# Kernel tuning notes

Measured on AMD Instinct MI355X. Metric: run time of the kernel, lower is better.

## Reference

```python
import jax, jax.numpy as jnp
import numpy as np

EPS = 1e-4
SILU_GAIN = 1.0 / 0.596  # magnitude-preserving SiLU gain
SCALES = (4, 4, 8)       # prod == A_DIM == 128
T = 0.3                  # residual lerp weight


def mp_silu(x):
    return jax.nn.silu(x) * SILU_GAIN


def pixel_norm(x):
    # normalize over channel dim (axis=1) to unit RMS
    return x * jax.lax.rsqrt(jnp.mean(jnp.square(x), axis=1, keepdims=True) + EPS)


def norm_w(w):
    # magnitude-preserving conv: per-output-filter L2-normalized weight
    n = jnp.sqrt(jnp.sum(jnp.square(w), axis=tuple(range(1, w.ndim)), keepdims=True) + 1e-8)
    return w / n


def mp_add(a, b, t=T):
    return (a * (1.0 - t) + b * t) / np.sqrt((1.0 - t) ** 2 + t ** 2)


def conv2d(x, w, groups=1, padding=((0, 0), (0, 0))):
    return jax.lax.conv_general_dilated(
        x, w, (1, 1), padding,
        dimension_numbers=('NCHW', 'OIHW', 'NCHW'), feature_group_count=groups)


def conv1d(x, w, groups=1, padding=((0, 0),)):
    return jax.lax.conv_general_dilated(
        x, w, (1,), padding,
        dimension_numbers=('NCH', 'OIH', 'NCH'), feature_group_count=groups)


def avgpool_freq(x, s):
    B, C, F, L = x.shape
    return jnp.mean(x.reshape(B, C, F // s, s, L), axis=3)


def min_gru(h, w):
    # minGRU: z_t = sigmoid(Wz h_t), c_t = Wc h_t, s_t = (1-z_t) s_{t-1} + z_t c_t
    z, c = jnp.split(conv1d(h, norm_w(w)), 2, axis=1)
    z = jax.nn.sigmoid(z)
    a, b = 1.0 - z, z * c  # linear recurrence s_t = a_t s_{t-1} + b_t

    def comb(x, y):
        a1, b1 = x
        a2, b2 = y
        return a2 * a1, a2 * b1 + b2

    _, out = jax.lax.associative_scan(comb, (a, b), axis=-1)
    return out


def conv_block(x, w1, wd, w2, wdn, s):
    # x: [B, d, F, L]
    x = pixel_norm(x)
    r = mp_silu(x)
    r = conv2d(r, norm_w(w1))                                            # d -> h, 1x1
    r = conv2d(r, norm_w(wd), groups=wd.shape[0], padding=((2, 2), (1, 1)))  # depthwise 5x3
    r = mp_silu(r)
    r = conv2d(r, norm_w(w2))                                            # h -> d, 1x1
    h = mp_add(x, r)
    return conv2d(avgpool_freq(h, s), norm_w(wdn))                       # d -> 2d, freq /s


def seq_block(x, hg_w, dw_w, gru_w, out_w):
    # x: [B, d, L]
    x = pixel_norm(x)
    h, g = jnp.split(conv1d(x, norm_w(hg_w)), 2, axis=1)  # each [B, H, L]
    h = mp_silu(h)
    h = conv1d(h, norm_w(dw_w), groups=dw_w.shape[0], padding=((1, 1),))  # depthwise k=3
    h = mp_silu(h)
    h = min_gru(h, gru_w)
    h = h * mp_silu(g)
    return mp_add(x, conv1d(h, norm_w(out_w)))


def setup_inputs() -> dict:
    key = jax.random.key(0)
    ks = jax.random.split(key, 18)
    rn = lambda k, s: jax.random.normal(k, s, dtype=jnp.float32)
    B, L, A = 2, 2048, 128
    return {
        'audio': rn(ks[0], (B, A, L)),
        'proj_w': rn(ks[1], (64, 1, 1, 1)) * 0.5,
        'proj_b': jnp.zeros((64,), jnp.float32),
        'c0_w1': rn(ks[2], (128, 64, 1, 1)),
        'c0_wd': rn(ks[3], (128, 1, 5, 3)),
        'c0_w2': rn(ks[4], (64, 128, 1, 1)),
        'c0_dn': rn(ks[5], (128, 64, 1, 1)),
        'c1_w1': rn(ks[6], (256, 128, 1, 1)),
        'c1_wd': rn(ks[7], (256, 1, 5, 3)),
        'c1_w2': rn(ks[8], (128, 256, 1, 1)),
        'c1_dn': rn(ks[9], (256, 128, 1, 1)),
        'c2_w1': rn(ks[10], (512, 256, 1, 1)),
        'c2_wd': rn(ks[11], (512, 1, 5, 3)),
        'c2_w2': rn(ks[12], (256, 512, 1, 1)),
        'c2_dn': rn(ks[13], (512, 256, 1, 1)),
        'hg_w': rn(ks[14], (4, 2048, 512, 1)),
        'dw_w': rn(ks[15], (4, 1024, 1, 3)),
        'gru_w': rn(ks[16], (4, 2048, 1024, 1)),
        'out_w': rn(ks[17], (4, 512, 1024, 1)),
    }


def reference(audio, proj_w, proj_b,
              c0_w1, c0_wd, c0_w2, c0_dn,
              c1_w1, c1_wd, c1_w2, c1_dn,
              c2_w1, c2_wd, c2_w2, c2_dn,
              hg_w, dw_w, gru_w, out_w):
    h = audio[:, None]  # [B, 1, A_DIM, L]
    h = conv2d(h, proj_w) + proj_b[None, :, None, None]
    blocks = ((c0_w1, c0_wd, c0_w2, c0_dn),
              (c1_w1, c1_wd, c1_w2, c1_dn),
              (c2_w1, c2_wd, c2_w2, c2_dn))
    for (w1, wd, w2, dn), s in zip(blocks, SCALES):
        h = conv_block(h, w1, wd, w2, dn, s)
    h = h[:, :, 0, :]  # freq dim reduced to 1 -> [B, dim, L]
    for i in range(hg_w.shape[0]):
        h = seq_block(h, hg_w[i], dw_w[i], gru_w[i], out_w[i])
    return mp_silu(h)
```

## Files before the change

### kernel.cpp

```cpp
#include <hip/hip_runtime.h>
#include <math.h>

#define GAIN 1.6778523489932886f
#define MPS  1.3130643285972254f

typedef __attribute__((ext_vector_type(8))) short short8;
typedef __attribute__((ext_vector_type(4))) short short4v;
typedef __attribute__((ext_vector_type(4))) float float4v;

__device__ __forceinline__ float silu_g(float x){
  float s = 1.0f/(1.0f + __expf(-x));
  return x*s*GAIN;
}
__device__ __forceinline__ short f2bf(float f){
  unsigned u = __builtin_bit_cast(unsigned, f);
  u += 0x7fffu + ((u >> 16) & 1u);
  return (short)(u >> 16);
}
__device__ __forceinline__ float bf2f(unsigned short h){
  return __builtin_bit_cast(float, ((unsigned)h) << 16);
}

typedef __attribute__((address_space(3))) unsigned int as3_uint;
typedef const __attribute__((address_space(1))) unsigned int as1_cuint;
__device__ __forceinline__ void gload16(const unsigned short* gsrc, unsigned short* ldst){
  __builtin_amdgcn_global_load_lds((as1_cuint*)gsrc, (as3_uint*)ldst, 16, 0, 0);
}

struct NcEnt { const float* w; int O, K, dstOff; };
struct NcArgs { NcEnt e[16]; };

__global__ __launch_bounds__(64) void normcast_kernel(NcArgs na, unsigned short* __restrict__ wbf){
  int row = blockIdx.x;
  int base = 0; int i;
  for (i = 0; i < 16; i++){
    if (row < base + na.e[i].O) break;
    base += na.e[i].O;
  }
  if (i >= 16) return;
  int r = row - base; int K = na.e[i].K;
  const float* w = na.e[i].w + (long)r*K;
  unsigned short* dst = wbf + na.e[i].dstOff + (long)r*K;
  int tid = threadIdx.x;
  float s = 0.f;
  const bool v4 = ((K & 3) == 0);
  if (v4){
    for (int k = tid*4; k < K; k += 256){
      float4v v = *(const float4v*)&w[k];
      s += v[0]*v[0] + v[1]*v[1] + v[2]*v[2] + v[3]*v[3];
    }
  } else {
    for (int k = tid; k < K; k += 64){ float v = w[k]; s += v*v; }
  }
  for (int off = 32; off; off >>= 1) s += __shfl_down(s, off);
  float inv = rsqrtf(__shfl(s, 0) + 1e-8f);
  if (v4){
    for (int k = tid*4; k < K; k += 256){
      float4v v = *(const float4v*)&w[k];
      short4v o = { f2bf(v[0]*inv), f2bf(v[1]*inv), f2bf(v[2]*inv), f2bf(v[3]*inv) };
      *(short4v*)&dst[k] = o;
    }
  } else {
    for (int k = tid; k < K; k += 64) dst[k] = (unsigned short)f2bf(w[k]*inv);
  }
}

__global__ __launch_bounds__(64) void projstats_kernel(const float* __restrict__ pw, const float* __restrict__ pb,
                                                       float* __restrict__ S){
  int t = threadIdx.x;
  float p = pw[t], q = pb[t];
  float s1 = p*p, s2 = p*q, s3 = q*q;
  for (int off = 32; off; off >>= 1){
    s1 += __shfl_down(s1, off); s2 += __shfl_down(s2, off); s3 += __shfl_down(s3, off);
  }
  if (t == 0){ S[0] = s1; S[1] = s2; S[2] = s3; }
}

__global__ __launch_bounds__(256) void invn_audio_kernel(const float* __restrict__ audio, const float* __restrict__ S,
                                                         float* __restrict__ invn){
  long i = blockIdx.x*256 + threadIdx.x;
  if (i >= (2L*128*2048)/4) return;
  long e = i*4;
  float S1 = S[0], S2 = S[1], S3 = S[2];
  float4v a = *(const float4v*)&audio[e];
  float4v o;
  #pragma unroll
  for (int j = 0; j < 4; j++) o[j] = rsqrtf((a[j]*a[j]*S1 + 2.f*a[j]*S2 + S3)/64.f + 1e-4f);
  *(float4v*)&invn[e] = o;
}

template<int G, bool BF>
__global__ __launch_bounds__(256) void invn_reduce_kernel(const void* __restrict__ Xv, float* __restrict__ invn,
                                                          int C, int F){
  constexpr int L = 256/G;
  int t = threadIdx.x; int cs = t / L; int li = t % L;
  long pos = (long)blockIdx.x*L + li;
  int bf = (int)(pos >> 11); int l = (int)(pos & 2047);
  int b = bf / F; int f = bf - b*F;
  long base = ((long)b*C*F + f)*2048 + l;
  long stride = (long)F*2048;
  float s = 0.f;
  if (BF){
    const unsigned short* X = (const unsigned short*)Xv;
    for (int c = cs; c < C; c += G){ float v = bf2f(X[base + (long)c*stride]); s += v*v; }
  } else {
    const float* X = (const float*)Xv;
    for (int c = cs; c < C; c += G){ float v = X[base + (long)c*stride]; s += v*v; }
  }
  __shared__ float red[256];
  red[t] = s; __syncthreads();
  #pragma unroll
  for (int off = G/2; off > 0; off >>= 1){
    if (cs < off) red[t] += red[t + off*L];
    __syncthreads();
  }
  if (cs == 0) invn[pos] = rsqrtf(red[li]/(float)C + 1e-4f);
}

template<bool SILU, bool BF>
__global__ __launch_bounds__(256) void applynorm_kernel(const void* __restrict__ Xv, const float* __restrict__ invn,
                                                        unsigned short* __restrict__ XB, int C, int F, long total4){
  long i = blockIdx.x*256 + threadIdx.x;
  if (i >= total4) return;
  long e = i*4;
  int l = (int)(e & 2047); long r = e >> 11;
  int f = (int)(r % F); long bc = r / F; int b = (int)(bc / C);
  float4v x;
  if (BF){
    short4v u = *(const short4v*)((const unsigned short*)Xv + e);
    x = (float4v){ bf2f((unsigned short)u[0]), bf2f((unsigned short)u[1]),
                   bf2f((unsigned short)u[2]), bf2f((unsigned short)u[3]) };
  } else {
    x = *(const float4v*)((const float*)Xv + e);
  }
  float4v iv = *(const float4v*)&invn[((long)b*F + f)*2048 + l];
  short4v o;
  #pragma unroll
  for (int j = 0; j < 4; j++){
    float v = x[j]*iv[j];
    o[j] = f2bf(SILU ? silu_g(v) : v);
  }
  *(short4v*)&XB[e] = o;
}

__global__ __launch_bounds__(256) void normT_kernel(const float* __restrict__ SEQ,
                                                    const float* __restrict__ invn,
                                                    unsigned short* __restrict__ XST){
  __shared__ float tile[64][65];
  const int l0 = blockIdx.x*64, c0 = blockIdx.y*64, b = blockIdx.z;
  const int t = threadIdx.x;
  const int lr = (t & 15)*4;
  const int cr = t >> 4;
  #pragma unroll
  for (int p = 0; p < 4; p++){
    int c = cr + p*16;
    float4v v = *(const float4v*)&SEQ[((long)(b*512 + c0 + c))*2048 + l0 + lr];
    tile[c][lr+0] = v[0]; tile[c][lr+1] = v[1]; tile[c][lr+2] = v[2]; tile[c][lr+3] = v[3];
  }
  __syncthreads();
  const int cc = (t & 7)*8;
  const int lw = t >> 3;
  #pragma unroll
  for (int p = 0; p < 2; p++){
    int l = lw + p*32;
    float iv = invn[b*2048 + l0 + l];
    short8 o;
    #pragma unroll
    for (int j = 0; j < 8; j++) o[j] = f2bf(tile[cc+j][l] * iv);
    *(short8*)&XST[((long)(b*2048 + l0 + l))*512 + c0 + cc] = o;
  }
}

struct GTArgs {
  const unsigned short* A;
  const unsigned short* B;
  unsigned short* O1;
  unsigned short* O2;
  int N, K;
};

template<int EMODE>
__global__ __launch_bounds__(256,2) void gemmT_kernel(GTArgs g){
  __shared__ __align__(16) char SMEMraw[49152];
  unsigned short (*Asm)[4096] = (unsigned short (*)[4096])SMEMraw;
  unsigned short (*Bsm)[4096] = (unsigned short (*)[4096])(SMEMraw + 24576);
  const int t = threadIdx.x;
  const int lane = t & 63;
  const int wc = (t >> 7) & 1;
  const int wsd = (t >> 6) & 1;
  const int q = lane >> 4, r16 = lane & 15;
  const int m0 = blockIdx.x * 128;
  const int n0 = blockIdx.y * 128;
  const int K = g.K;

  const int r0 = t >> 2;
  const int c8 = (((t & 3) ^ ((r0 >> 1) & 3)) << 3);
  const unsigned short* Ap = g.A + (long)(n0 + r0)*K + c8;
  const unsigned short* Bp = g.B + (long)(m0 + r0)*K + c8;

  auto stage = [&](int bi, int k0){
    gload16(Ap + k0,           &Asm[bi][t*8]);
    gload16(Ap + 64*K + k0,    &Asm[bi][2048 + t*8]);
    gload16(Bp + k0,           &Bsm[bi][t*8]);
    gload16(Bp + 64*K + k0,    &Bsm[bi][2048 + t*8]);
  };

  float4v acc[4][4];
  #pragma unroll
  for (int i = 0; i < 4; i++)
    #pragma unroll
    for (int j = 0; j < 4; j++) acc[i][j] = (float4v){0.f,0.f,0.f,0.f};

  const int nit = K >> 5;
  stage(0, 0);
  stage(1, 32);

  const int qsw = ((q ^ ((r16 >> 1) & 3)) << 3);

  for (int it = 0; it < nit; ++it){
    if (it + 2 < nit){
      stage((it + 2) % 3, (it + 2) << 5);
      asm volatile("" ::: "memory");
      asm volatile("s_waitcnt vmcnt(8)" ::: "memory");
    } else if (it + 1 < nit){
      asm volatile("s_waitcnt vmcnt(4)" ::: "memory");
    } else {
      asm volatile("s_waitcnt vmcnt(0)" ::: "memory");
    }
    __builtin_amdgcn_s_barrier();
    asm volatile("" ::: "memory");

    const unsigned short* As = Asm[it % 3];
    const unsigned short* Bs = Bsm[it % 3];
    short8 afr[4], bfr[4];
    #pragma unroll
    for (int i = 0; i < 4; i++) afr[i] = *(const short8*)&As[(wc*64 + i*16 + r16)*32 + qsw];
    #pragma unroll
    for (int j = 0; j < 4; j++) bfr[j] = *(const short8*)&Bs[(wsd*64 + j*16 + r16)*32 + qsw];
    #pragma unroll
    for (int i = 0; i < 4; i++)
      #pragma unroll
      for (int j = 0; j < 4; j++)
        acc[i][j] = __builtin_amdgcn_mfma_f32_16x16x32_bf16(afr[i], bfr[j], acc[i][j], 0, 0, 0);

    asm volatile("" ::: "memory");
    __builtin_amdgcn_s_barrier();
  }

  if (EMODE == 1 && n0 < 1024){
    float* Cf = (float*)SMEMraw;
    #pragma unroll
    for (int h = 0; h < 2; h++){
      __syncthreads();
      if (wc == h){
        #pragma unroll
        for (int j = 0; j < 4; j++){
          int m = wsd*64 + j*16 + r16;
          #pragma unroll
          for (int i = 0; i < 4; i++)
            *(float4v*)&Cf[m*68 + i*16 + q*4] = acc[i][j];
        }
      }
      __syncthreads();
      #pragma unroll
      for (int p = 0; p < 4; p++){
        int m = (t >> 3) + p*32;
        int n8 = (t & 7)*8;
        int gm = m0 + m; int b = gm >> 11, l = gm & 2047;
        float4v v0 = *(const float4v*)&Cf[m*68 + n8];
        float4v v1 = *(const float4v*)&Cf[m*68 + n8 + 4];
        short8 o;
        #pragma unroll
        for (int e = 0; e < 4; e++){ o[e] = f2bf(silu_g(v0[e])); o[e+4] = f2bf(silu_g(v1[e])); }
        *(short8*)&g.O1[((long)(b*2048 + l))*1024 + (n0 + h*64 + n8)] = o;
      }
    }
  } else {
    float* Csm = (float*)SMEMraw;
    #pragma unroll
    for (int qtr = 0; qtr < 4; qtr++){
      __syncthreads();
      if (wc == (qtr >> 1)){
        #pragma unroll
        for (int ii = 0; ii < 2; ii++){
          int i = (qtr & 1)*2 + ii;
          #pragma unroll
          for (int j = 0; j < 4; j++){
            int m = wsd*64 + j*16 + r16;
            #pragma unroll
            for (int rg = 0; rg < 4; rg++)
              Csm[(ii*16 + q*4 + rg)*132 + m] = acc[i][j][rg];
          }
        }
      }
      __syncthreads();
      #pragma unroll
      for (int sp = 0; sp < 2; sp++){
        int nrow = (t >> 4) + sp*16;
        int n = n0 + qtr*32 + nrow;
        int m8 = (t & 15)*8;
        int gm = m0 + m8; int b = gm >> 11, l = gm & 2047;
        float4v v0 = *(const float4v*)&Csm[nrow*132 + m8];
        float4v v1 = *(const float4v*)&Csm[nrow*132 + m8 + 4];
        short8 o;
        #pragma unroll
        for (int e = 0; e < 4; e++){ o[e] = f2bf(v0[e]); o[e+4] = f2bf(v1[e]); }
        if (EMODE == 1) *(short8*)&g.O2[((long)(b*1024 + (n - 1024)))*2048 + l] = o;
        else            *(short8*)&g.O1[((long)(b*2048 + n))*2048 + l] = o;
      }
    }
  }
}

struct GemmArgs {
  const unsigned short* A;
  const unsigned short* Bh;
  const float* invn; const float* audio;
  const float* pw; const float* pb;
  const unsigned short* auxXH;
  unsigned short* CoutH; unsigned short* Cout2H;
  int N, K, Fdim, Lw, lq0, BLw, Bl0, CLw, Cl0, Nsto, Fsrc;
};

template<int BMODE, int EMODE>
__global__ __launch_bounds__(256,2) void mgemm_kernel(GemmArgs g){
  __shared__ __align__(16) char SMEMraw[20480];
  unsigned short* Asm = (unsigned short*)SMEMraw;
  unsigned short* Bsm = Asm + 128*40;
  const int t = threadIdx.x;
  const int lane = t & 63;
  const int wave = t >> 6;
  const int wc = wave >> 1, wsd = wave & 1;
  const int q = lane >> 4, r16 = lane & 15;
  const int s0 = blockIdx.x * 128;
  const int n0 = blockIdx.y * 128;
  const int FL = g.Fdim * g.Lw;

  const int ar = t >> 1, ah = t & 1;
  const int an = n0 + ar;
  const bool aval = an < g.N;
  const unsigned short* Aptr = g.A + (long)an*g.K + ah*16;

  const int kg = t & 7, mg = t >> 3;
  const int mb = s0 + mg*4;
  int bcol = mb / FL; int rr = mb - bcol*FL;
  int fcol = (g.Fdim > 1) ? (rr / g.Lw) : 0;
  int labs = g.lq0 + (rr - fcol*g.Lw);
  const bool cv = (bcol < 2);
  bool lv[4];
  #pragma unroll
  for (int j = 0; j < 4; j++) lv[j] = cv && (labs + j >= 0) && (labs + j < 2048);
  const bool vec4 = cv && (labs >= 0) && (labs + 3 < 2048);
  const unsigned short* bbase = g.Bh;
  if (cv) bbase = g.Bh + ((long)(bcol*g.K)*g.Fsrc + fcol)*g.BLw + (labs - g.Bl0);
  const long kstep = (long)g.Fsrc * g.BLw;

  float invn4[4] = {0,0,0,0}, aud4[4] = {0,0,0,0};
  if (BMODE == 2){
    #pragma unroll
    for (int j = 0; j < 4; j++) if (lv[j]){
      invn4[j] = g.invn[(bcol*g.Fdim + fcol)*2048 + labs + j];
      aud4[j]  = g.audio[(bcol*128 + fcol)*2048 + labs + j];
    }
  }

  float4v acc[4][4];
  #pragma unroll
  for (int i = 0; i < 4; i++)
    #pragma unroll
    for (int j = 0; j < 4; j++) acc[i][j] = (float4v){0.f,0.f,0.f,0.f};

  short8 pa0 = {0,0,0,0,0,0,0,0}, pa1 = {0,0,0,0,0,0,0,0};
  short4v praw[4];
  #pragma unroll
  for (int i = 0; i < 4; i++) praw[i] = (short4v){0,0,0,0};

  auto ldA = [&](int kb){
    if (aval){
      pa0 = *(const short8*)(Aptr + kb);
      pa1 = *(const short8*)(Aptr + kb + 8);
    }
  };
  auto ldB = [&](int kb){
    #pragma unroll
    for (int i = 0; i < 4; i++){
      const int k = kb + kg*4 + i;
      const unsigned short* bp = bbase + (long)k*kstep;
      if (vec4) praw[i] = *(const short4v*)bp;
      else {
        short4v u = {0,0,0,0};
        #pragma unroll
        for (int j = 0; j < 4; j++) if (lv[j]) u[j] = (short)bp[j];
        praw[i] = u;
      }
    }
  };

  ldA(0);
  if (BMODE == 0) ldB(0);

  for (int k0 = 0; k0 < g.K; k0 += 32){
    short8 sa0 = pa0, sa1 = pa1;
    short4v bpk[4];
    if (BMODE == 0){
      #pragma unroll
      for (int j = 0; j < 4; j++){
        short4v p;
        #pragma unroll
        for (int i = 0; i < 4; i++) p[i] = praw[i][j];
        bpk[j] = p;
      }
    } else {
      float tv[4][4];
      #pragma unroll
      for (int i = 0; i < 4; i++){
        const int k = k0 + kg*4 + i;
        const float pwk = g.pw[k], pbk = g.pb[k];
        #pragma unroll
        for (int j = 0; j < 4; j++) tv[i][j] = lv[j] ? silu_g((aud4[j]*pwk + pbk)*invn4[j]) : 0.f;
      }
      #pragma unroll
      for (int j = 0; j < 4; j++){
        short4v p;
        #pragma unroll
        for (int i = 0; i < 4; i++) p[i] = f2bf(tv[i][j]);
        bpk[j] = p;
      }
    }
    if (k0 + 32 < g.K){
      ldA(k0 + 32);
      if (BMODE == 0) ldB(k0 + 32);
    }

    __syncthreads();
    *(short8*)&Asm[ar*40 + ah*16]     = sa0;
    *(short8*)&Asm[ar*40 + ah*16 + 8] = sa1;
    #pragma unroll
    for (int j = 0; j < 4; j++)
      *(short4v*)&Bsm[(mg*4 + j)*40 + kg*4] = bpk[j];
    __syncthreads();

    short8 afr[4], bfr[4];
    #pragma unroll
    for (int i = 0; i < 4; i++) afr[i] = *(const short8*)&Asm[(wc*64 + i*16 + r16)*40 + q*8];
    #pragma unroll
    for (int j = 0; j < 4; j++) bfr[j] = *(const short8*)&Bsm[(wsd*64 + j*16 + r16)*40 + q*8];
    #pragma unroll
    for (int i = 0; i < 4; i++)
      #pragma unroll
      for (int j = 0; j < 4; j++)
        acc[i][j] = __builtin_amdgcn_mfma_f32_16x16x32_bf16(afr[i], bfr[j], acc[i][j], 0, 0, 0);
  }

  {
    float* Csm = (float*)SMEMraw;
    #pragma unroll
    for (int qtr = 0; qtr < 4; qtr++){
      __syncthreads();
      if (wc == (qtr >> 1)){
        #pragma unroll
        for (int ii = 0; ii < 2; ii++){
          int i = (qtr & 1)*2 + ii;
          #pragma unroll
          for (int j = 0; j < 4; j++){
            int m = wsd*64 + j*16 + r16;
            #pragma unroll
            for (int rg = 0; rg < 4; rg++)
              Csm[(ii*16 + q*4 + rg)*132 + m] = acc[i][j][rg];
          }
        }
      }
      __syncthreads();
      #pragma unroll
      for (int sp = 0; sp < 2; sp++){
        int nrow = (t >> 4) + sp*16;
        int n = n0 + qtr*32 + nrow;
        int m8 = (t & 15)*8;
        if (n >= g.N) continue;
        int sg = s0 + m8;
        int b2 = sg / FL; int r2 = sg - b2*FL;
        if (b2 >= 2) continue;
        int f2 = (g.Fdim > 1) ? (r2 / g.Lw) : 0;
        int l2 = g.lq0 + (r2 - f2*g.Lw);
        float4v v0 = *(const float4v*)&Csm[nrow*132 + m8];
        float4v v1 = *(const float4v*)&Csm[nrow*132 + m8 + 4];
        long obase = ((long)(b2*g.Nsto + n)*g.Fdim + f2)*g.CLw + (l2 - g.Cl0);
        short8 o;
        if (EMODE == 1){
          #pragma unroll
          for (int e = 0; e < 4; e++){ o[e] = f2bf(v0[e]); o[e+4] = f2bf(v1[e]); }
        } else if (EMODE == 2){
          short8 axv = *(const short8*)&g.auxXH[((long)(b2*g.N + n)*g.Fdim + f2)*2048 + l2];
          const float* ivp = &g.invn[(b2*g.Fdim + f2)*2048 + l2];
          float4v iv0 = *(const float4v*)ivp;
          float4v iv1 = *(const float4v*)(ivp + 4);
          #pragma unroll
          for (int e = 0; e < 4; e++){
            float xn0 = bf2f((unsigned short)axv[e]) * iv0[e];
            float xn1 = bf2f((unsigned short)axv[e+4]) * iv1[e];
            o[e]   = f2bf((xn0*0.7f + v0[e]*0.3f)*MPS);
            o[e+4] = f2bf((xn1*0.7f + v1[e]*0.3f)*MPS);
          }
        } else {
          float pwn = g.pw[n], pbn = g.pb[n];
          const float* ap  = &g.audio[(b2*128 + f2)*2048 + l2];
          const float* ivp = &g.invn[(b2*g.Fdim + f2)*2048 + l2];
          float4v a0 = *(const float4v*)ap,  a1 = *(const float4v*)(ap + 4);
          float4v iv0 = *(const float4v*)ivp, iv1 = *(const float4v*)(ivp + 4);
          #pragma unroll
          for (int e = 0; e < 4; e++){
            float xn0 = (a0[e]*pwn + pbn)*iv0[e];
            float xn1 = (a1[e]*pwn + pbn)*iv1[e];
            o[e]   = f2bf((xn0*0.7f + v0[e]*0.3f)*MPS);
            o[e+4] = f2bf((xn1*0.7f + v1[e]*0.3f)*MPS);
          }
        }
        *(short8*)&g.CoutH[obase] = o;
      }
    }
  }
}

struct DnArgs {
  const unsigned short* A; const unsigned short* P;
  float* Cout; unsigned short* CoutH;
  int N, K, F2, Lc, l0;
};

template<int EMODE>
__global__ __launch_bounds__(256,4) void mgemm64_kernel(DnArgs g){
  __shared__ __align__(16) char SMEM[10240];
  unsigned short* Asm = (unsigned short*)SMEM;
  unsigned short* Bsm = Asm + 64*40;
  const int t = threadIdx.x;
  const int lane = t & 63;
  const int wave = t >> 6;
  const int wc = wave >> 1, wsd = wave & 1;
  const int q = lane >> 4, r16 = lane & 15;
  const int s0 = blockIdx.x * 64;
  const int n0 = blockIdx.y * 64;
  const int FL = g.F2 * g.Lc;

  const int ar = t >> 2, ah = t & 3;
  const unsigned short* Aptr = g.A + (long)(n0 + ar)*g.K + ah*8;
  const int kg = t & 7, mg = t >> 3;
  const bool bstage = (mg < 16);
  const int mb = s0 + (mg & 15)*4;
  const int bcol = mb / FL; const int rr = mb - bcol*FL;
  const int fcol = rr / g.Lc; const int li = rr - fcol*g.Lc;
  const unsigned short* bbase = g.P + ((long)(bcol*g.K)*g.F2 + fcol)*g.Lc + li;
  const long kstep = (long)g.F2 * g.Lc;

  float4v acc[2][2];
  #pragma unroll
  for (int i = 0; i < 2; i++)
    #pragma unroll
    for (int j = 0; j < 2; j++) acc[i][j] = (float4v){0.f,0.f,0.f,0.f};

  short8 pa = {0,0,0,0,0,0,0,0};
  short4v praw[4];
  #pragma unroll
  for (int i = 0; i < 4; i++) praw[i] = (short4v){0,0,0,0};

  auto ldA = [&](int kb){ pa = *(const short8*)(Aptr + kb); };
  auto ldB = [&](int kb){
    if (bstage){
      #pragma unroll
      for (int i = 0; i < 4; i++)
        praw[i] = *(const short4v*)(bbase + (long)(kb + kg*4 + i)*kstep);
    }
  };
  ldA(0); ldB(0);

  for (int k0 = 0; k0 < g.K; k0 += 32){
    short8 sa = pa;
    short4v bpk[4];
    #pragma unroll
    for (int j = 0; j < 4; j++){
      short4v p;
      #pragma unroll
      for (int i = 0; i < 4; i++) p[i] = praw[i][j];
      bpk[j] = p;
    }
    if (k0 + 32 < g.K){ ldA(k0 + 32); ldB(k0 + 32); }

    __syncthreads();
    *(short8*)&Asm[ar*40 + ah*8] = sa;
    if (bstage){
      #pragma unroll
      for (int j = 0; j < 4; j++)
        *(short4v*)&Bsm[((mg & 15)*4 + j)*40 + kg*4] = bpk[j];
    }
    __syncthreads();

    short8 afr[2], bfr[2];
    #pragma unroll
    for (int i = 0; i < 2; i++) afr[i] = *(const short8*)&Asm[(wc*32 + i*16 + r16)*40 + q*8];
    #pragma unroll
    for (int j = 0; j < 2; j++) bfr[j] = *(const short8*)&Bsm[(wsd*32 + j*16 + r16)*40 + q*8];
    #pragma unroll
    for (int i = 0; i < 2; i++)
      #pragma unroll
      for (int j = 0; j < 2; j++)
        acc[i][j] = __builtin_amdgcn_mfma_f32_16x16x32_bf16(afr[i], bfr[j], acc[i][j], 0, 0, 0);
  }

  {
    float* Csm = (float*)SMEM;
    const int b2 = s0 / FL; const int r20 = s0 - b2*FL;
    const int f2c = r20 / g.Lc; const int l2c = g.l0 + (r20 - f2c*g.Lc);
    #pragma unroll
    for (int nq = 0; nq < 4; nq++){
      __syncthreads();
      if (wc == (nq >> 1)){
        const int i = nq & 1;
        #pragma unroll
        for (int j = 0; j < 2; j++)
          #pragma unroll
          for (int rg = 0; rg < 4; rg++)
            Csm[(q*4 + rg)*68 + wsd*32 + j*16 + r16] = acc[i][j][rg];
      }
      __syncthreads();
      int nrow = t >> 4;
      int mq = (t & 15)*4;
      int n = n0 + nq*16 + nrow;
      float4v v = *(const float4v*)&Csm[nrow*68 + mq];
      long oidx = ((long)(b2*g.N + n)*g.F2 + f2c)*2048 + l2c + mq;
      if (EMODE == 0){
        *(float4v*)&g.Cout[oidx] = v;
      } else {
        short4v o = { f2bf(v[0]), f2bf(v[1]), f2bf(v[2]), f2bf(v[3]) };
        *(short4v*)&g.CoutH[oidx] = o;
      }
    }
  }
}

template<int EMODE>
__global__ __launch_bounds__(256,4) void seqout_kernel(const unsigned short* __restrict__ A,
                                                       const unsigned short* __restrict__ Bh,
                                                       const float* __restrict__ invn,
                                                       const float* __restrict__ auxX,
                                                       float* __restrict__ Cout, int K){
  __shared__ __align__(16) char SMEM[10240];
  unsigned short* Asm = (unsigned short*)SMEM;
  unsigned short* Bsm = Asm + 64*40;
  const int t = threadIdx.x;
  const int lane = t & 63;
  const int wave = t >> 6;
  const int wc = wave >> 1, wsd = wave & 1;
  const int q = lane >> 4, r16 = lane & 15;
  const int s0 = blockIdx.x * 64;
  const int n0 = blockIdx.y * 64;

  const int ar = t >> 2, ah = t & 3;
  const unsigned short* Aptr = A + (long)(n0 + ar)*K + ah*8;
  const int kg = t & 7, mg = t >> 3;
  const bool bstage = (mg < 16);
  const int mb = s0 + (mg & 15)*4;
  const int bcol = mb >> 11, lb = mb & 2047;
  const unsigned short* bbase = Bh + ((long)bcol*K)*2048 + lb;

  float4v acc[2][2];
  #pragma unroll
  for (int i = 0; i < 2; i++)
    #pragma unroll
    for (int j = 0; j < 2; j++) acc[i][j] = (float4v){0.f,0.f,0.f,0.f};

  short8 pa = {0,0,0,0,0,0,0,0};
  short4v praw[4];
  #pragma unroll
  for (int i = 0; i < 4; i++) praw[i] = (short4v){0,0,0,0};

  auto ldA = [&](int kb){ pa = *(const short8*)(Aptr + kb); };
  auto ldB = [&](int kb){
    if (bstage){
      #pragma unroll
      for (int i = 0; i < 4; i++)
        praw[i] = *(const short4v*)(bbase + (long)(kb + kg*4 + i)*2048);
    }
  };
  ldA(0); ldB(0);

  for (int k0 = 0; k0 < K; k0 += 32){
    short8 sa = pa;
    short4v bpk[4];
    #pragma unroll
    for (int j = 0; j < 4; j++){
      short4v p;
      #pragma unroll
      for (int i = 0; i < 4; i++) p[i] = praw[i][j];
      bpk[j] = p;
    }
    if (k0 + 32 < K){ ldA(k0 + 32); ldB(k0 + 32); }

    __syncthreads();
    *(short8*)&Asm[ar*40 + ah*8] = sa;
    if (bstage){
      #pragma unroll
      for (int j = 0; j < 4; j++)
        *(short4v*)&Bsm[((mg & 15)*4 + j)*40 + kg*4] = bpk[j];
    }
    __syncthreads();

    short8 afr[2], bfr[2];
    #pragma unroll
    for (int i = 0; i < 2; i++) afr[i] = *(const short8*)&Asm[(wc*32 + i*16 + r16)*40 + q*8];
    #pragma unroll
    for (int j = 0; j < 2; j++) bfr[j] = *(const short8*)&Bsm[(wsd*32 + j*16 + r16)*40 + q*8];
    #pragma unroll
    for (int i = 0; i < 2; i++)
      #pragma unroll
      for (int j = 0; j < 2; j++)
        acc[i][j] = __builtin_amdgcn_mfma_f32_16x16x32_bf16(afr[i], bfr[j], acc[i][j], 0, 0, 0);
  }

  {
    float* Csm = (float*)SMEM;
    const int b2 = s0 >> 11; const int l0b = s0 & 2047;
    #pragma unroll
    for (int nq = 0; nq < 4; nq++){
      __syncthreads();
      if (wc == (nq >> 1)){
        const int i = nq & 1;
        #pragma unroll
        for (int j = 0; j < 2; j++)
          #pragma unroll
          for (int rg = 0; rg < 4; rg++)
            Csm[(q*4 + rg)*68 + wsd*32 + j*16 + r16] = acc[i][j][rg];
      }
      __syncthreads();
      int nrow = t >> 4;
      int mq = (t & 15)*4;
      int n = n0 + nq*16 + nrow;
      int l = l0b + mq;
      float4v v = *(const float4v*)&Csm[nrow*68 + mq];
      float4v ax = *(const float4v*)&auxX[((long)b2*512 + n)*2048 + l];
      float4v iv = *(const float4v*)&invn[b2*2048 + l];
      float4v r;
      #pragma unroll
      for (int e = 0; e < 4; e++){
        float xn = ax[e]*iv[e];
        float rr = (xn*0.7f + v[e]*0.3f)*MPS;
        r[e] = (EMODE == 6) ? silu_g(rr) : rr;
      }
      *(float4v*)&Cout[((long)b2*512 + n)*2048 + l] = r;
    }
  }
}

__global__ __launch_bounds__(256) void poolf_kernel(const unsigned short* __restrict__ Hb,
                                                    unsigned short* __restrict__ P,
                                                    int F2, int s, int Lc, long total4){
  long i = blockIdx.x*256 + threadIdx.x;
  if (i >= total4) return;
  long e = i*4;
  int li = (int)(e % Lc); long r0 = e / Lc;
  int f2 = (int)(r0 % F2); long r = r0 / F2;
  const unsigned short* src = Hb + ((long)r*F2*s + (long)f2*s)*Lc + li;
  float a0=0,a1=0,a2=0,a3=0;
  for (int p = 0; p < s; p++){
    short4v u = *(const short4v*)(src + (long)p*Lc);
    a0 += bf2f((unsigned short)u[0]); a1 += bf2f((unsigned short)u[1]);
    a2 += bf2f((unsigned short)u[2]); a3 += bf2f((unsigned short)u[3]);
  }
  float inv = 1.f/(float)s;
  short4v o = { f2bf(a0*inv), f2bf(a1*inv), f2bf(a2*inv), f2bf(a3*inv) };
  *(short4v*)&P[((long)r*F2 + f2)*Lc + li] = o;
}

struct DwArgs { const unsigned short* R1; const unsigned short* wd; unsigned short* R2; int C, F, Lc, l0; };
__global__ __launch_bounds__(256) void dw2d_kernel(DwArgs a){
  int idx = blockIdx.x*256 + threadIdx.x;
  int Lq = a.Lc >> 3;
  int Fq = a.F >> 2;
  int total = 2*a.C*Fq*Lq;
  if (idx >= total) return;
  int lq = idx % Lq; int r = idx / Lq;
  int fq = r % Fq; r /= Fq;
  int c = r % a.C; int b = r / a.C;
  int f0 = fq*4;
  int labs = a.l0 + lq*8;
  int Lw = a.Lc + 8;
  const unsigned short* base = a.R1 + (long)((b*a.C + c)*a.F)*Lw + (labs - (a.l0 - 4));
  const unsigned short* w = a.wd + c*15;
  float W[5][3];
  #pragma unroll
  for (int tp = 0; tp < 5; tp++)
    #pragma unroll
    for (int j = 0; j < 3; j++) W[tp][j] = bf2f(w[tp*3 + j]);

  const bool llo = (labs > 0);
  const bool lhi = (labs + 8 < 2048);
  float acc[4][8];
  #pragma unroll
  for (int t = 0; t < 4; t++)
    #pragma unroll
    for (int j = 0; j < 8; j++) acc[t][j] = 0.f;

  #pragma unroll
  for (int r8 = 0; r8 < 8; r8++){
    int rrow = f0 - 2 + r8;
    if (rrow < 0 || rrow >= a.F) continue;
    const unsigned short* p = base + (long)rrow*Lw;
    short4v u0 = *(const short4v*)p;
    short4v u1 = *(const short4v*)(p + 4);
    float x[10];
    x[0] = llo ? bf2f(p[-1]) : 0.f;
    x[1] = bf2f((unsigned short)u0[0]); x[2] = bf2f((unsigned short)u0[1]);
    x[3] = bf2f((unsigned short)u0[2]); x[4] = bf2f((unsigned short)u0[3]);
    x[5] = bf2f((unsigned short)u1[0]); x[6] = bf2f((unsigned short)u1[1]);
    x[7] = bf2f((unsigned short)u1[2]); x[8] = bf2f((unsigned short)u1[3]);
    x[9] = lhi ? bf2f(p[8]) : 0.f;
    #pragma unroll
    for (int t = 0; t < 4; t++){
      const int df = r8 - 2 - t;
      if (df < -2 || df > 2) continue;
      float w0 = W[df+2][0], w1 = W[df+2][1], w2 = W[df+2][2];
      #pragma unroll
      for (int j = 0; j < 8; j++)
        acc[t][j] += w0*x[j] + w1*x[j+1] + w2*x[j+2];
    }
  }

  unsigned short* ob = a.R2 + ((long)((b*a.C + c)*a.F + f0))*a.Lc + (labs - a.l0);
  #pragma unroll
  for (int t = 0; t < 4; t++){
    short8 o;
    #pragma unroll
    for (int j = 0; j < 8; j++) o[j] = f2bf(silu_g(acc[t][j]));
    *(short8*)(ob + (long)t*a.Lc) = o;
  }
}

__global__ __launch_bounds__(256) void dwseqT_kernel(const unsigned short* __restrict__ HST,
                                                     const unsigned short* __restrict__ w,
                                                     unsigned short* __restrict__ H2T){
  int idx = blockIdx.x*256 + threadIdx.x;
  if (idx >= 2*2048*128) return;
  int c0 = (idx & 127) * 8; long bt = idx >> 7;
  int tt = (int)(bt & 2047);
  const unsigned short* base = HST + bt*1024 + c0;
  short8 zz = {0,0,0,0,0,0,0,0};
  short8 x1 = *(const short8*)base;
  short8 x0 = (tt > 0)    ? *(const short8*)(base - 1024) : zz;
  short8 x2 = (tt < 2047) ? *(const short8*)(base + 1024) : zz;
  const unsigned short* wp = w + c0*3;
  short8 o;
  #pragma unroll
  for (int j = 0; j < 8; j++){
    float w0 = bf2f(wp[3*j]), w1 = bf2f(wp[3*j+1]), w2 = bf2f(wp[3*j+2]);
    float v = w0*bf2f((unsigned short)x0[j]) + w1*bf2f((unsigned short)x1[j]) + w2*bf2f((unsigned short)x2[j]);
    o[j] = f2bf(silu_g(v));
  }
  *(short8*)&H2T[bt*1024 + c0] = o;
}

__global__ __launch_bounds__(256) void scan_kernel(const unsigned short* __restrict__ ZC, const unsigned short* __restrict__ G,
                                                   unsigned short* __restrict__ SC){
  int bc = blockIdx.x;
  int b = bc >> 10, c = bc & 1023;
  const unsigned short* zrow = ZC + ((long)(b*2048 + c))*2048;
  const unsigned short* crow = ZC + ((long)(b*2048 + 1024 + c))*2048;
  const unsigned short* grow = G + (long)bc*2048;
  unsigned short* orow = SC + (long)bc*2048;
  int tid = threadIdx.x;
  int t0 = tid*8;
  short8 zv = *(const short8*)&zrow[t0];
  short8 cv = *(const short8*)&crow[t0];
  float av[8], bv[8];
  float A = 1.f, Bv = 0.f;
  #pragma unroll
  for (int j = 0; j < 8; j++){
    float z = bf2f((unsigned short)zv[j]); float cval = bf2f((unsigned short)cv[j]);
    float zs = 1.f/(1.f + __expf(-z));
    float a = 1.f - zs; float bb = zs*cval;
    av[j] = a; bv[j] = bb;
    Bv = a*Bv + bb;
    A = a*A;
  }
  int lane = tid & 63, wv = tid >> 6;
  float iA = A, iB = Bv;
  #pragma unroll
  for (int off = 1; off < 64; off <<= 1){
    float pA = __shfl_up(iA, off);
    float pB = __shfl_up(iB, off);
    if (lane >= off){ iB = iA*pB + iB; iA = iA*pA; }
  }
  float exA = __shfl_up(iA, 1);
  float exB = __shfl_up(iB, 1);
  if (lane == 0){ exA = 1.f; exB = 0.f; }
  __shared__ float sWA[4], sWB[4];
  if (lane == 63){ sWA[wv] = iA; sWB[wv] = iB; }
  __syncthreads();
  float wpA = 1.f, wpB = 0.f;
  #pragma unroll
  for (int w = 0; w < 3; w++){
    if (w < wv){ wpB = sWA[w]*wpB + sWB[w]; wpA = wpA*sWA[w]; }
  }
  float h = exA*wpB + exB;
  short8 gv = *(const short8*)&grow[t0];
  short8 ov;
  #pragma unroll
  for (int j = 0; j < 8; j++){
    h = av[j]*h + bv[j];
    ov[j] = f2bf(h * silu_g(bf2f((unsigned short)gv[j])));
  }
  *(short8*)&orow[t0] = ov;
}

extern "C" void kernel_launch(void* const* d_in, const int* in_sizes, int n_in,
                              void* d_out, int out_size, void* d_ws, size_t ws_size,
                              hipStream_t stream) {
  const float* audio = (const float*)d_in[0];
  const float* pw = (const float*)d_in[1];
  const float* pb = (const float*)d_in[2];
  const float* cw1[3] = {(const float*)d_in[3], (const float*)d_in[7], (const float*)d_in[11]};
  const float* cwd[3] = {(const float*)d_in[4], (const float*)d_in[8], (const float*)d_in[12]};
  const float* cw2[3] = {(const float*)d_in[5], (const float*)d_in[9], (const float*)d_in[13]};
  const float* cdn[3] = {(const float*)d_in[6], (const float*)d_in[10], (const float*)d_in[14]};
  const float* hgw  = (const float*)d_in[15];
  const float* dww  = (const float*)d_in[16];
  const float* gruw = (const float*)d_in[17];
  const float* outw = (const float*)d_in[18];
  float* out = (float*)d_out;

  char* P0 = (char*)d_ws;
  float*          INVW = (float*)P0;                    P0 += 131072;
  unsigned short* WBF  = (unsigned short*)P0;           P0 += 30443776;
  float*          INVN = (float*)P0;                    P0 += 2097152;
  char*           XBZC = P0;                            P0 += 33554432;
  unsigned short* IN1h = (unsigned short*)P0;           P0 += 33554432;
  unsigned short* IN2h = (unsigned short*)P0;           P0 += 16777216;
  float*          SEQ  = (float*)P0;                    P0 += 8388608;
  char*           ARENA = P0;
  long arenaBytes = (long)ws_size - (long)(P0 - (char*)d_ws);
  float* S = INVW + 32000;

  const float* wsrc[16] = {cw1[0],cwd[0],cw2[0],cdn[0], cw1[1],cwd[1],cw2[1],cdn[1],
                           cw1[2],cwd[2],cw2[2],cdn[2], hgw, dww, gruw, outw};
  int Os[16] = {128,128,64,128, 256,256,128,256, 512,512,256,512, 8192,4096,8192,2048};
  int Ks[16] = {64,15,128,64, 128,15,256,128, 256,15,512,256, 512,3,1024,1024};
  int wbfOff[16];
  {
    int wo = 0;
    for (int i = 0; i < 16; i++){ wbfOff[i] = wo; wo += Os[i]*Ks[i]; }
  }
  {
    NcArgs na;
    int rows = 0;
    for (int i = 0; i < 16; i++){
      na.e[i].w = wsrc[i]; na.e[i].O = Os[i]; na.e[i].K = Ks[i]; na.e[i].dstOff = wbfOff[i];
      rows += Os[i];
    }
    normcast_kernel<<<rows, 64, 0, stream>>>(na, WBF);
  }
  projstats_kernel<<<1, 64, 0, stream>>>(pw, pb, S);

  int Cin_[3]  = {64,128,256};
  int Cmid_[3] = {128,256,512};
  int F_[3]    = {128,32,8};
  int s_[3]    = {4,4,8};
  const unsigned short* XinH[3] = {nullptr, IN1h, IN2h};
  unsigned short* XoutH[3] = {IN1h, IN2h, nullptr};
  int iW1[3]={0,4,8}, iWd[3]={1,5,9}, iW2[3]={2,6,10}, iDn[3]={3,7,11};

  for (int b = 0; b < 3; b++){
    int Cin = Cin_[b], Cmid = Cmid_[b], F = F_[b], s = s_[b];
    int F2 = F/s;
    int nc = 16;
    for (int c = 1; c <= 16; c <<= 1){
      long Lc = 2048/c;
      long bytes = 2L*(2L*Cmid*F*(Lc+8) + 2L*Cmid*F*Lc + 2L*Cin*F*Lc + 2L*Cin*F2*Lc);
      if (bytes <= arenaBytes){ nc = c; break; }
    }
    int Lc = 2048/nc;
    unsigned short* R1 = (unsigned short*)ARENA;
    unsigned short* R2 = R1 + 2L*Cmid*F*(Lc+8);
    unsigned short* Hb = R2 + 2L*Cmid*F*Lc;
    unsigned short* Pb = Hb + 2L*Cin*F*Lc;
    unsigned short* XB = (unsigned short*)XBZC;

    if (b == 0){
      invn_audio_kernel<<<(2*128*2048/4+255)/256, 256, 0, stream>>>(audio, S, INVN);
    } else {
      int positions = 2*F*2048;
      invn_reduce_kernel<8,true><<<positions/32, 256, 0, stream>>>(XinH[b], INVN, Cin, F);
      long total4 = (long)2*Cin*F*2048/4;
      applynorm_kernel<true,true><<<(int)((total4+255)/256), 256, 0, stream>>>(XinH[b], INVN, XB, Cin, F, total4);
    }

    for (int ci = 0; ci < nc; ci++){
      int l0 = ci*Lc;
      GemmArgs ga{};
      ga.A = WBF + wbfOff[iW1[b]];
      ga.Bh = XB; ga.invn = INVN; ga.audio = audio; ga.pw = pw; ga.pb = pb;
      ga.CoutH = R1; ga.N = Cmid; ga.K = Cin; ga.Fdim = F; ga.Lw = Lc+8; ga.lq0 = l0-4;
      ga.BLw = 2048; ga.Bl0 = 0; ga.CLw = Lc+8; ga.Cl0 = l0-4; ga.Nsto = Cmid; ga.Fsrc = F;
      int M1 = 2*F*(Lc+8);
      dim3 g1((M1+127)/128, (Cmid+127)/128);
      if (b == 0) mgemm_kernel<2,1><<<g1,256,0,stream>>>(ga);
      else        mgemm_kernel<0,1><<<g1,256,0,stream>>>(ga);
      DwArgs da{R1, WBF + wbfOff[iWd[b]], R2, Cmid, F, Lc, l0};
      int tdw = 2*Cmid*(F/4)*(Lc/8);
      dw2d_kernel<<<(tdw+255)/256, 256, 0, stream>>>(da);
      GemmArgs gb{};
      gb.A = WBF + wbfOff[iW2[b]];
      gb.Bh = R2; gb.invn = INVN; gb.audio = audio; gb.pw = pw; gb.pb = pb; gb.auxXH = XinH[b];
      gb.CoutH = Hb; gb.N = Cin; gb.K = Cmid; gb.Fdim = F; gb.Lw = Lc; gb.lq0 = l0;
      gb.BLw = Lc; gb.Bl0 = l0; gb.CLw = Lc; gb.Cl0 = l0; gb.Nsto = Cin; gb.Fsrc = F;
      int M2 = 2*F*Lc;
      dim3 g2((M2+127)/128, (Cin+127)/128);
      if (b == 0) mgemm_kernel<0,3><<<g2,256,0,stream>>>(gb);
      else        mgemm_kernel<0,2><<<g2,256,0,stream>>>(gb);
      long tp4 = (2L*Cin*F2*Lc)/4;
      poolf_kernel<<<(int)((tp4+255)/256), 256, 0, stream>>>(Hb, Pb, F2, s, Lc, tp4);
      DnArgs dn{};
      dn.A = WBF + wbfOff[iDn[b]]; dn.P = Pb;
      dn.Cout = SEQ; dn.CoutH = XoutH[b];
      dn.N = Cmid; dn.K = Cin; dn.F2 = F2; dn.Lc = Lc; dn.l0 = l0;
      dim3 gdn((2*F2*Lc)/64, Cmid/64);
      if (b == 2) mgemm64_kernel<0><<<gdn,256,0,stream>>>(dn);
      else        mgemm64_kernel<1><<<gdn,256,0,stream>>>(dn);
    }
  }

  unsigned short* XST = IN1h;
  unsigned short* HST = XST + 2097152;
  unsigned short* G   = HST + 4194304;
  unsigned short* H2T = G  + 4194304;
  unsigned short* SC  = H2T + 4194304;
  unsigned short* ZCh = (unsigned short*)XBZC;

  for (int i = 0; i < 4; i++){
    invn_reduce_kernel<16,false><<<4096/16, 256, 0, stream>>>(SEQ, INVN, 512, 1);
    normT_kernel<<<dim3(32,8,2), 256, 0, stream>>>(SEQ, INVN, XST);
    GTArgs gh{ WBF + wbfOff[12] + (long)i*2048*512, XST, HST, G, 2048, 512 };
    gemmT_kernel<1><<<dim3(32,16), 256, 0, stream>>>(gh);
    dwseqT_kernel<<<2048, 256, 0, stream>>>(HST, WBF + wbfOff[13] + i*1024*3, H2T);
    GTArgs gz{ WBF + wbfOff[14] + (long)i*2048*1024, H2T, ZCh, nullptr, 2048, 1024 };
    gemmT_kernel<0><<<dim3(32,16), 256, 0, stream>>>(gz);
    scan_kernel<<<2048,256,0,stream>>>(ZCh, G, SC);
    const unsigned short* oA = WBF + wbfOff[15] + (long)i*512*1024;
    if (i < 3) seqout_kernel<5><<<dim3(64,8),256,0,stream>>>(oA, SC, INVN, SEQ, SEQ, 1024);
    else       seqout_kernel<6><<<dim3(64,8),256,0,stream>>>(oA, SC, INVN, SEQ, out, 1024);
  }

  (void)in_sizes; (void)n_in; (void)out_size;
}
```

Measured before the change: 1.107 ms.

## Use K-major transposed normalized input for first 1x1 conv GEMM in blocks 1-2

Adds a kernel that applies pixel-norm and SiLU to the block input and writes it transposed into a channel-contiguous, L-padded buffer. A new GEMM kernel reads this K-major layout with direct 16-byte global-to-LDS loads in a three-stage pipeline, replacing the generic mgemm path for blocks 1 and 2 when the arena can hold the extra buffer. The aim is faster B-operand staging and less index arithmetic in the expand conv. The cost is an extra transposed buffer in the arena, which may force more L-chunks.

```diff
diff --git a/kernel.cpp b/kernel.cpp
--- a/kernel.cpp
+++ b/kernel.cpp
@@ -171,6 +171,49 @@
   }
 }
 
+__global__ __launch_bounds__(256) void normxT_kernel(const unsigned short* __restrict__ X,
+                                                     const float* __restrict__ invn,
+                                                     unsigned short* __restrict__ XBT,
+                                                     int C, int F){
+  __shared__ unsigned short tile[64][72];
+  const int bf = blockIdx.z;
+  const int b = bf / F, f = bf - b*F;
+  const int c0 = blockIdx.y * 64;
+  const int lA = blockIdx.x * 64 - 64;
+  const int t = threadIdx.x;
+  const int lr8 = (t & 7)*8, cr = t >> 3;
+  #pragma unroll
+  for (int p = 0; p < 2; p++){
+    int c = c0 + cr + p*32;
+    int labs = lA + lr8;
+    short8 v = {0,0,0,0,0,0,0,0};
+    if (labs >= 0 && labs < 2048){
+      short8 u = *(const short8*)&X[((long)(b*C + c)*F + f)*2048 + labs];
+      const float* ivp = &invn[((long)b*F + f)*2048 + labs];
+      float4v iv0 = *(const float4v*)ivp;
+      float4v iv1 = *(const float4v*)(ivp + 4);
+      #pragma unroll
+      for (int j = 0; j < 4; j++){
+        v[j]   = f2bf(silu_g(bf2f((unsigned short)u[j])   * iv0[j]));
+        v[j+4] = f2bf(silu_g(bf2f((unsigned short)u[j+4]) * iv1[j]));
+      }
+    }
+    *(short8*)&tile[cr + p*32][lr8] = v;
+  }
+  __syncthreads();
+  const int cc = (t & 7)*8, sw = t >> 3;
+  #pragma unroll
+  for (int p = 0; p < 2; p++){
+    int sl = sw + p*32;
+    int s = lA + sl + 4;
+    if (s < 0 || s >= 2056) continue;
+    short8 o;
+    #pragma unroll
+    for (int j = 0; j < 8; j++) o[j] = (short)tile[cc + j][sl];
+    *(short8*)&XBT[(((long)bf)*2056 + s)*C + c0 + cc] = o;
+  }
+}
+
 struct GTArgs {
   const unsigned short* A;
   const unsigned short* B;
@@ -307,6 +350,125 @@
         for (int e = 0; e < 4; e++){ o[e] = f2bf(v0[e]); o[e+4] = f2bf(v1[e]); }
         if (EMODE == 1) *(short8*)&g.O2[((long)(b*1024 + (n - 1024)))*2048 + l] = o;
         else            *(short8*)&g.O1[((long)(b*2048 + n))*2048 + l] = o;
+      }
+    }
+  }
+}
+
+struct GCArgs {
+  const unsigned short* A;
+  const unsigned short* XBT;
+  unsigned short* R1;
+  int N, K, F, Lc8, l0;
+};
+
+__global__ __launch_bounds__(256,2) void gemmC_kernel(GCArgs g){
+  __shared__ __align__(16) char SMEMraw[49152];
+  unsigned short (*Asm)[4096] = (unsigned short (*)[4096])SMEMraw;
+  unsigned short (*Bsm)[4096] = (unsigned short (*)[4096])(SMEMraw + 24576);
+  const int t = threadIdx.x;
+  const int lane = t & 63;
+  const int wc = (t >> 7) & 1;
+  const int wsd = (t >> 6) & 1;
+  const int q = lane >> 4, r16 = lane & 15;
+  const int m0 = blockIdx.x * 128;
+  const int n0 = blockIdx.y * 128;
+  const int K = g.K;
+  const int Lc8 = g.Lc8;
+  const int FLw = g.F * Lc8;
+
+  const int r0 = t >> 2;
+  const int c8 = (((t & 3) ^ ((r0 >> 1) & 3)) << 3);
+  const unsigned short* Ap = g.A + (long)(n0 + r0)*K + c8;
+  int mA = m0 + r0;
+  int bA = mA / FLw; int rA = mA - bA*FLw; int fA = rA / Lc8; int lA = rA - fA*Lc8;
+  const unsigned short* Bp0 = g.XBT + (((long)(bA*g.F + fA))*2056 + g.l0 + lA)*K + c8;
+  int mB = mA + 64;
+  int bB = mB / FLw; int rB = mB - bB*FLw; int fB = rB / Lc8; int lB = rB - fB*Lc8;
+  const unsigned short* Bp1 = g.XBT + (((long)(bB*g.F + fB))*2056 + g.l0 + lB)*K + c8;
+
+  auto stage = [&](int bi, int k0){
+    gload16(Ap + k0,        &Asm[bi][t*8]);
+    gload16(Ap + 64*K + k0, &Asm[bi][2048 + t*8]);
+    gload16(Bp0 + k0,       &Bsm[bi][t*8]);
+    gload16(Bp1 + k0,       &Bsm[bi][2048 + t*8]);
+  };
+
+  float4v acc[4][4];
+  #pragma unroll
+  for (int i = 0; i < 4; i++)
+    #pragma unroll
+    for (int j = 0; j < 4; j++) acc[i][j] = (float4v){0.f,0.f,0.f,0.f};
+
+  const int nit = K >> 5;
+  stage(0, 0);
+  stage(1, 32);
+
+  const int qsw = ((q ^ ((r16 >> 1) & 3)) << 3);
+
+  for (int it = 0; it < nit; ++it){
+    if (it + 2 < nit){
+      stage((it + 2) % 3, (it + 2) << 5);
+      asm volatile("" ::: "memory");
+      asm volatile("s_waitcnt vmcnt(8)" ::: "memory");
+    } else if (it + 1 < nit){
+      asm volatile("s_waitcnt vmcnt(4)" ::: "memory");
+    } else {
+      asm volatile("s_waitcnt vmcnt(0)" ::: "memory");
+    }
+    __builtin_amdgcn_s_barrier();
+    asm volatile("" ::: "memory");
+
+    const unsigned short* As = Asm[it % 3];
+    const unsigned short* Bs = Bsm[it % 3];
+    short8 afr[4], bfr[4];
+    #pragma unroll
+    for (int i = 0; i < 4; i++) afr[i] = *(const short8*)&As[(wc*64 + i*16 + r16)*32 + qsw];
+    #pragma unroll
+    for (int j = 0; j < 4; j++) bfr[j] = *(const short8*)&Bs[(wsd*64 + j*16 + r16)*32 + qsw];
+    #pragma unroll
+    for (int i = 0; i < 4; i++)
+      #pragma unroll
+      for (int j = 0; j < 4; j++)
+        acc[i][j] = __builtin_amdgcn_mfma_f32_16x16x32_bf16(afr[i], bfr[j], acc[i][j], 0, 0, 0);
+
+    asm volatile("" ::: "memory");
+    __builtin_amdgcn_s_barrier();
+  }
+
+  {
+    int m8 = (t & 15)*8;
+    int gm = m0 + m8;
+    int bo = gm / FLw; int ro = gm - bo*FLw; int fo = ro / Lc8; int lo = ro - fo*Lc8;
+    long obase0 = (((long)(bo*g.N) * g.F + fo))*Lc8 + lo;
+    float* Csm = (float*)SMEMraw;
+    #pragma unroll
+    for (int qtr = 0; qtr < 4; qtr++){
+      __syncthreads();
+      if (wc == (qtr >> 1)){
+        #pragma unroll
+        for (int ii = 0; ii < 2; ii++){
+          int i = (qtr & 1)*2 + ii;
+          #pragma unroll
+          for (int j = 0; j < 4; j++){
+            int m = wsd*64 + j*16 + r16;
+            #pragma unroll
+            for (int rg = 0; rg < 4; rg++)
+              Csm[(ii*16 + q*4 + rg)*132 + m] = acc[i][j][rg];
+          }
+        }
+      }
+      __syncthreads();
+      #pragma unroll
+      for (int sp = 0; sp < 2; sp++){
+        int nrow = (t >> 4) + sp*16;
+        int n = n0 + qtr*32 + nrow;
+        float4v v0 = *(const float4v*)&Csm[nrow*132 + m8];
+        float4v v1 = *(const float4v*)&Csm[nrow*132 + m8 + 4];
+        short8 o;
+        #pragma unroll
+        for (int e = 0; e < 4; e++){ o[e] = f2bf(v0[e]); o[e+4] = f2bf(v1[e]); }
+        *(short8*)&g.R1[obase0 + (long)n*g.F*Lc8] = o;
       }
     }
   }
@@ -968,14 +1130,28 @@
   for (int b = 0; b < 3; b++){
     int Cin = Cin_[b], Cmid = Cmid_[b], F = F_[b], s = s_[b];
     int F2 = F/s;
-    int nc = 16;
-    for (int c = 1; c <= 16; c <<= 1){
-      long Lc = 2048/c;
-      long bytes = 2L*(2L*Cmid*F*(Lc+8) + 2L*Cmid*F*Lc + 2L*Cin*F*Lc + 2L*Cin*F2*Lc);
-      if (bytes <= arenaBytes){ nc = c; break; }
+
+    bool kmajor = false;
+    int nc = 0;
+    long xbtE = 2L*F*2056*Cin;
+    if (b > 0){
+      for (int c = 1; c <= 16; c <<= 1){
+        long Lc_ = 2048/c;
+        long bytes = 2L*(2L*Cmid*F*(Lc_+8) + 2L*Cmid*F*Lc_ + 2L*Cin*F*Lc_ + 2L*Cin*F2*Lc_ + xbtE);
+        if (bytes <= arenaBytes){ nc = c; kmajor = true; break; }
+      }
+    }
+    if (!kmajor){
+      nc = 16;
+      for (int c = 1; c <= 16; c <<= 1){
+        long Lc_ = 2048/c;
+        long bytes = 2L*(2L*Cmid*F*(Lc_+8) + 2L*Cmid*F*Lc_ + 2L*Cin*F*Lc_ + 2L*Cin*F2*Lc_);
+        if (bytes <= arenaBytes){ nc = c; break; }
+      }
     }
     int Lc = 2048/nc;
-    unsigned short* R1 = (unsigned short*)ARENA;
+    unsigned short* XBT = (unsigned short*)ARENA;
+    unsigned short* R1 = kmajor ? (XBT + xbtE) : (unsigned short*)ARENA;
     unsigned short* R2 = R1 + 2L*Cmid*F*(Lc+8);
     unsigned short* Hb = R2 + 2L*Cmid*F*Lc;
     unsigned short* Pb = Hb + 2L*Cin*F*Lc;
@@ -986,21 +1162,39 @@
     } else {
       int positions = 2*F*2048;
       invn_reduce_kernel<8,true><<<positions/32, 256, 0, stream>>>(XinH[b], INVN, Cin, F);
-      long total4 = (long)2*Cin*F*2048/4;
-      applynorm_kernel<true,true><<<(int)((total4+255)/256), 256, 0, stream>>>(XinH[b], INVN, XB, Cin, F, total4);
+      if (kmajor){
+        normxT_kernel<<<dim3(34, Cin/64, 2*F), 256, 0, stream>>>(XinH[b], INVN, XBT, Cin, F);
+      } else {
+        long total4 = (long)2*Cin*F*2048/4;
+        applynorm_kernel<true,true><<<(int)((total4+255)/256), 256, 0, stream>>>(XinH[b], INVN, XB, Cin, F, total4);
+      }
     }
 
     for (int ci = 0; ci < nc; ci++){
       int l0 = ci*Lc;
-      GemmArgs ga{};
-      ga.A = WBF + wbfOff[iW1[b]];
-      ga.Bh = XB; ga.invn = INVN; ga.audio = audio; ga.pw = pw; ga.pb = pb;
-      ga.CoutH = R1; ga.N = Cmid; ga.K = Cin; ga.Fdim = F; ga.Lw = Lc+8; ga.lq0 = l0-4;
-      ga.BLw = 2048; ga.Bl0 = 0; ga.CLw = Lc+8; ga.Cl0 = l0-4; ga.Nsto = Cmid; ga.Fsrc = F;
-      int M1 = 2*F*(Lc+8);
-      dim3 g1((M1+127)/128, (Cmid+127)/128);
-      if (b == 0) mgemm_kernel<2,1><<<g1,256,0,stream>>>(ga);
-      else        mgemm_kernel<0,1><<<g1,256,0,stream>>>(ga);
+      if (b == 0){
+        GemmArgs ga{};
+        ga.A = WBF + wbfOff[iW1[b]];
+        ga.Bh = XB; ga.invn = INVN; ga.audio = audio; ga.pw = pw; ga.pb = pb;
+        ga.CoutH = R1; ga.N = Cmid; ga.K = Cin; ga.Fdim = F; ga.Lw = Lc+8; ga.lq0 = l0-4;
+        ga.BLw = 2048; ga.Bl0 = 0; ga.CLw = Lc+8; ga.Cl0 = l0-4; ga.Nsto = Cmid; ga.Fsrc = F;
+        int M1 = 2*F*(Lc+8);
+        dim3 g1((M1+127)/128, (Cmid+127)/128);
+        mgemm_kernel<2,1><<<g1,256,0,stream>>>(ga);
+      } else if (kmajor){
+        GCArgs gc{ WBF + wbfOff[iW1[b]], XBT, R1, Cmid, Cin, F, Lc+8, l0 };
+        dim3 g1((2*F*(Lc+8))/128, Cmid/128);
+        gemmC_kernel<<<g1,256,0,stream>>>(gc);
+      } else {
+        GemmArgs ga{};
+        ga.A = WBF + wbfOff[iW1[b]];
+        ga.Bh = XB; ga.invn = INVN; ga.audio = audio; ga.pw = pw; ga.pb = pb;
+        ga.CoutH = R1; ga.N = Cmid; ga.K = Cin; ga.Fdim = F; ga.Lw = Lc+8; ga.lq0 = l0-4;
+        ga.BLw = 2048; ga.Bl0 = 0; ga.CLw = Lc+8; ga.Cl0 = l0-4; ga.Nsto = Cmid; ga.Fsrc = F;
+        int M1 = 2*F*(Lc+8);
+        dim3 g1((M1+127)/128, (Cmid+127)/128);
+        mgemm_kernel<0,1><<<g1,256,0,stream>>>(ga);
+      }
       DwArgs da{R1, WBF + wbfOff[iWd[b]], R2, Cmid, F, Lc, l0};
       int tdw = 2*Cmid*(F/4)*(Lc/8);
       dw2d_kernel<<<(tdw+255)/256, 256, 0, stream>>>(da);
```

New measurement: 1.089 ms. About the same (-1.6%).
